# Optimization experiments

Measured on AMD Instinct MI355X. Metric: run time of the kernel, lower is better.

The kernel has to match this reference:

```python
import jax, jax.numpy as jnp
import numpy as np


def setup_inputs() -> dict:
    key = jax.random.key(0)
    k1, k2, k3 = jax.random.split(key, 3)
    B, L, H = 4, 4096, 1024
    x = jax.random.normal(k1, (B, L, H), dtype=jnp.float32)
    # 0.02 scale keeps attention logits in a sane range (like trained weights)
    in_proj_weight = jax.random.normal(k2, (3 * H, H), dtype=jnp.float32) * 0.02
    in_proj_bias = jnp.zeros((3 * H,), dtype=jnp.float32)
    out_proj_weight = jax.random.normal(k3, (H, H), dtype=jnp.float32) * 0.02
    out_proj_bias = jnp.zeros((H,), dtype=jnp.float32)
    return {
        "x": x,
        "in_proj_weight": in_proj_weight,
        "in_proj_bias": in_proj_bias,
        "out_proj_weight": out_proj_weight,
        "out_proj_bias": out_proj_bias,
        "num_heads": 16,
        "window_size": 128,
    }


def _windowed_mha(x, in_proj_weight, in_proj_bias, out_proj_weight, out_proj_bias,
                  num_heads, window_size):
    B, L, H = x.shape
    P = window_size
    pad = (-L) % P  # static
    xp = jnp.pad(x, ((0, 0), (0, pad), (0, 0))) if pad else x
    Lp = xp.shape[1]
    nw = Lp // P
    w = xp.reshape(B * nw, P, H)  # [NW, P, H]
    # packed QKV projection (torch MHA: q,k,v = split(x @ W_in.T + b_in))
    qkv = jnp.einsum('nph,dh->npd', w, in_proj_weight) + in_proj_bias
    q, k, v = jnp.split(qkv, 3, axis=-1)
    hd = H // num_heads

    def to_heads(t):
        return t.reshape(B * nw, P, num_heads, hd).transpose(0, 2, 1, 3)  # [NW, Hh, P, hd]

    q, k, v = to_heads(q), to_heads(k), to_heads(v)
    scale = 1.0 / jnp.sqrt(jnp.asarray(hd, dtype=x.dtype))
    scores = jnp.einsum('nhqd,nhkd->nhqk', q * scale, k)  # [NW, Hh, P, P]
    attn = jax.nn.softmax(scores, axis=-1)
    o = jnp.einsum('nhqk,nhkd->nhqd', attn, v)  # [NW, Hh, P, hd]
    o = o.transpose(0, 2, 1, 3).reshape(B * nw, P, H)
    o = jnp.einsum('nph,oh->npo', o, out_proj_weight) + out_proj_bias
    o = o.reshape(B, Lp, H)
    return o[:, :L]


def reference(x, in_proj_weight, in_proj_bias, out_proj_weight, out_proj_bias,
              num_heads, window_size):
    return _windowed_mha(x, in_proj_weight, in_proj_bias, out_proj_weight,
                         out_proj_bias, num_heads, window_size)
```

## Files before the change

### kernel.cpp

```cpp
#include <hip/hip_runtime.h>
#include <hip/hip_bf16.h>
#include <cstdint>


typedef __bf16 bf16_t;
typedef __bf16 bf16x8 __attribute__((ext_vector_type(8)));
typedef __bf16 bf16x4 __attribute__((ext_vector_type(4)));
typedef float  floatx4 __attribute__((ext_vector_type(4)));

#define MFMA_16x16x32(A, B, C) __builtin_amdgcn_mfma_f32_16x16x32_bf16(A, B, C, 0, 0, 0)

__device__ __forceinline__ void gld_lds16(const bf16_t* g, bf16_t* l) {
  __builtin_amdgcn_global_load_lds(
      (__attribute__((address_space(1))) void*)(void*)(g),
      (__attribute__((address_space(3))) void*)(l), 16, 0, 0);
}

__global__ void cvt_f32_to_bf16(const float* __restrict__ src,
                                bf16_t* __restrict__ dst, int n8) {
  int i = blockIdx.x * blockDim.x + threadIdx.x;
  if (i >= n8) return;
  const float4* s4 = (const float4*)src;
  float4 a = s4[2 * (size_t)i];
  float4 b = s4[2 * (size_t)i + 1];
  bf16x8 o;
  o[0] = (bf16_t)a.x; o[1] = (bf16_t)a.y; o[2] = (bf16_t)a.z; o[3] = (bf16_t)a.w;
  o[4] = (bf16_t)b.x; o[5] = (bf16_t)b.y; o[6] = (bf16_t)b.z; o[7] = (bf16_t)b.w;
  *(bf16x8*)(dst + (size_t)i * 8) = o;
}

__global__ void cvt_repack_win(const float* __restrict__ Win,
                               bf16_t* __restrict__ Wpk) {
  const int dr = blockIdx.x;
  const int head = dr / 192, s = dr - head * 192;
  const int src = (s < 64) ? head * 64 + s
                : (s < 128) ? 1024 + head * 64 + (s - 64)
                            : 2048 + head * 64 + (s - 128);
  const float4* srow = (const float4*)(Win + (size_t)src * 1024);
  const int i = threadIdx.x;
  float4 a = srow[2 * i];
  float4 b = srow[2 * i + 1];
  bf16x8 o;
  o[0] = (bf16_t)a.x; o[1] = (bf16_t)a.y; o[2] = (bf16_t)a.z; o[3] = (bf16_t)a.w;
  o[4] = (bf16_t)b.x; o[5] = (bf16_t)b.y; o[6] = (bf16_t)b.z; o[7] = (bf16_t)b.w;
  *(bf16x8*)(Wpk + (size_t)dr * 1024 + i * 8) = o;
}

template <bool F32OUT>
__global__ __launch_bounds__(256, 3) void gemm_bt(
    const bf16_t* __restrict__ A, const bf16_t* __restrict__ Bm,
    const float* __restrict__ bias, void* __restrict__ Cp,
    int M, int N, int K) {
  __shared__ bf16_t As[128 * 64];
  __shared__ bf16_t Bs[128 * 64];
  const int tid  = threadIdx.x;
  const int lane = tid & 63;
  const int wave = tid >> 6;
  const int n16  = lane & 15;
  const int q4   = lane >> 4;
  const int wm   = (wave >> 1) * 64;
  const int wn   = (wave & 1) * 64;
  const int m0   = blockIdx.y * 128;
  const int n0   = blockIdx.x * 128;

  floatx4 acc[4][4] = {};

  for (int k0 = 0; k0 < K; k0 += 64) {
    __syncthreads();
#pragma unroll
    for (int it = 0; it < 4; ++it) {
      const int ch = it * 256 + tid;
      const int r  = ch >> 3;
      const int c8 = (ch & 7) ^ (r & 7);
      gld_lds16(A  + (size_t)(m0 + r) * K + k0 + c8 * 8,
                As + (it * 256 + wave * 64) * 8);
      gld_lds16(Bm + (size_t)(n0 + r) * K + k0 + c8 * 8,
                Bs + (it * 256 + wave * 64) * 8);
    }
    __syncthreads();

#pragma unroll
    for (int half = 0; half < 2; ++half) {
      bf16x8 af[4], bfr[4];
#pragma unroll
      for (int i = 0; i < 4; ++i) {
        const int row = wm + i * 16 + n16;
        af[i] = *(const bf16x8*)&As[row * 64 + (((half * 4 + q4) ^ (row & 7)) * 8)];
      }
#pragma unroll
      for (int j = 0; j < 4; ++j) {
        const int row = wn + j * 16 + n16;
        bfr[j] = *(const bf16x8*)&Bs[row * 64 + (((half * 4 + q4) ^ (row & 7)) * 8)];
      }
#pragma unroll
      for (int i = 0; i < 4; ++i)
#pragma unroll
        for (int j = 0; j < 4; ++j)
          acc[i][j] = MFMA_16x16x32(af[i], bfr[j], acc[i][j]);
    }
  }

#pragma unroll
  for (int i = 0; i < 4; ++i)
#pragma unroll
    for (int j = 0; j < 4; ++j) {
      const int col = n0 + wn + j * 16 + n16;
      const float b = bias[col];
#pragma unroll
      for (int r = 0; r < 4; ++r) {
        const int row = m0 + wm + i * 16 + q4 * 4 + r;
        const float v = acc[i][j][r] + b;
        if (F32OUT)
          ((float*)Cp)[(size_t)row * N + col] = v;
        else
          ((bf16_t*)Cp)[(size_t)row * N + col] = (bf16_t)v;
      }
    }
}

__global__ __launch_bounds__(256, 3) void qkv_attn(
    const bf16_t* __restrict__ X,
    const bf16_t* __restrict__ Wpk,
    const float* __restrict__ bin,
    bf16_t* __restrict__ o)
{
  __shared__ bf16_t smem[26624];
  bf16_t* Xs  = smem;
  bf16_t* Ws  = smem + 8192;
  bf16_t* qs  = smem;
  bf16_t* ks  = smem + 9216;
  bf16_t* vsT = smem + 18432;
  bf16_t* Ps  = smem;

  const int wid  = blockIdx.x;
  const int h    = blockIdx.y;
  const int tid  = threadIdx.x;
  const int lane = tid & 63;
  const int wave = tid >> 6;
  const int n16  = lane & 15;
  const int q4   = lane >> 4;
  const int wm   = (wave >> 1) * 64;
  const int wn   = (wave & 1) * 96;

  const bf16_t* Xg = X + (size_t)wid * 128 * 1024;
  const bf16_t* Wg = Wpk + (size_t)h * 192 * 1024;

  floatx4 acc[4][6] = {};
  for (int k0 = 0; k0 < 1024; k0 += 64) {
    __syncthreads();
#pragma unroll
    for (int it = 0; it < 4; ++it) {
      const int ch = it * 256 + tid;
      const int r  = ch >> 3;
      const int c8 = (ch & 7) ^ (r & 7);
      gld_lds16(Xg + (size_t)r * 1024 + k0 + c8 * 8,
                Xs + (it * 256 + wave * 64) * 8);
    }
#pragma unroll
    for (int it = 0; it < 6; ++it) {
      const int ch = it * 256 + tid;
      const int r  = ch >> 3;
      const int c8 = (ch & 7) ^ (r & 7);
      gld_lds16(Wg + (size_t)r * 1024 + k0 + c8 * 8,
                Ws + (it * 256 + wave * 64) * 8);
    }
    __syncthreads();

#pragma unroll
    for (int half = 0; half < 2; ++half) {
      bf16x8 af[4], bfr[6];
#pragma unroll
      for (int i = 0; i < 4; ++i) {
        const int row = wm + i * 16 + n16;
        af[i] = *(const bf16x8*)&Xs[row * 64 + (((half * 4 + q4) ^ (row & 7)) * 8)];
      }
#pragma unroll
      for (int j = 0; j < 6; ++j) {
        const int row = wn + j * 16 + n16;
        bfr[j] = *(const bf16x8*)&Ws[row * 64 + (((half * 4 + q4) ^ (row & 7)) * 8)];
      }
#pragma unroll
      for (int i = 0; i < 4; ++i)
#pragma unroll
        for (int j = 0; j < 6; ++j)
          acc[i][j] = MFMA_16x16x32(af[i], bfr[j], acc[i][j]);
    }
  }
  __syncthreads();

#pragma unroll
  for (int j = 0; j < 6; ++j) {
    const int base = wn + j * 16;
    const int col  = base + n16;
    const int gb = (base < 64) ? h * 64 + col
                 : (base < 128) ? 1024 + h * 64 + (col - 64)
                                : 2048 + h * 64 + (col - 128);
    const float bias = bin[gb];
#pragma unroll
    for (int i = 0; i < 4; ++i) {
      const int row0 = wm + i * 16 + q4 * 4;
      if (base < 64) {
#pragma unroll
        for (int r = 0; r < 4; ++r)
          qs[(row0 + r) * 72 + col] = (bf16_t)((acc[i][j][r] + bias) * 0.125f);
      } else if (base < 128) {
#pragma unroll
        for (int r = 0; r < 4; ++r)
          ks[(row0 + r) * 72 + (col - 64)] = (bf16_t)(acc[i][j][r] + bias);
      } else {
        bf16x4 pv;
#pragma unroll
        for (int r = 0; r < 4; ++r) pv[r] = (bf16_t)(acc[i][j][r] + bias);
        const int d = col - 128;
        const int c8 = row0 >> 3, pos = row0 & 7;
        *(bf16x4*)&vsT[d * 128 + ((c8 ^ n16) << 3) + pos] = pv;
      }
    }
  }
  __syncthreads();

  floatx4 sacc[2][8] = {};
#pragma unroll
  for (int ks0 = 0; ks0 < 2; ++ks0) {
    bf16x8 aq[2];
#pragma unroll
    for (int i = 0; i < 2; ++i)
      aq[i] = *(const bf16x8*)&qs[(wave * 32 + i * 16 + n16) * 72 + ks0 * 32 + q4 * 8];
#pragma unroll
    for (int j = 0; j < 8; ++j) {
      bf16x8 bk = *(const bf16x8*)&ks[(j * 16 + n16) * 72 + ks0 * 32 + q4 * 8];
      sacc[0][j] = MFMA_16x16x32(aq[0], bk, sacc[0][j]);
      sacc[1][j] = MFMA_16x16x32(aq[1], bk, sacc[1][j]);
    }
  }
  __syncthreads();

  float invs[2][4];
#pragma unroll
  for (int i = 0; i < 2; ++i) {
#pragma unroll
    for (int r = 0; r < 4; ++r) {
      float vals[8];
      float s = 0.f;
#pragma unroll
      for (int j = 0; j < 8; ++j) {
        vals[j] = __expf(sacc[i][j][r]);
        s += vals[j];
      }
      for (int m = 1; m < 16; m <<= 1) s += __shfl_xor(s, m, 64);
      invs[i][r] = 1.0f / s;
      const int prow = wave * 32 + i * 16 + q4 * 4 + r;
#pragma unroll
      for (int j = 0; j < 8; ++j)
        Ps[prow * 136 + j * 16 + n16] = (bf16_t)vals[j];
    }
  }
  __syncthreads();

  floatx4 oacc[2][4] = {};
#pragma unroll
  for (int kk = 0; kk < 4; ++kk) {
    bf16x8 ap[2];
#pragma unroll
    for (int i = 0; i < 2; ++i)
      ap[i] = *(const bf16x8*)&Ps[(wave * 32 + i * 16 + n16) * 136 + kk * 32 + q4 * 8];
#pragma unroll
    for (int j = 0; j < 4; ++j) {
      const int d = j * 16 + n16;
      bf16x8 bv = *(const bf16x8*)&vsT[d * 128 + (((kk * 4 + q4) ^ n16) << 3)];
      oacc[0][j] = MFMA_16x16x32(ap[0], bv, oacc[0][j]);
      oacc[1][j] = MFMA_16x16x32(ap[1], bv, oacc[1][j]);
    }
  }

  bf16_t* go = o + (size_t)wid * 128 * 1024 + h * 64;
#pragma unroll
  for (int i = 0; i < 2; ++i)
#pragma unroll
    for (int j = 0; j < 4; ++j)
#pragma unroll
      for (int r = 0; r < 4; ++r) {
        const int row = wave * 32 + i * 16 + q4 * 4 + r;
        go[(size_t)row * 1024 + j * 16 + n16] = (bf16_t)(oacc[i][j][r] * invs[i][r]);
      }
}

extern "C" void kernel_launch(void* const* d_in, const int* in_sizes, int n_in,
                              void* d_out, int out_size, void* d_ws, size_t ws_size,
                              hipStream_t stream) {
  const float* x    = (const float*)d_in[0];
  const float* Win  = (const float*)d_in[1];
  const float* bin  = (const float*)d_in[2];
  const float* Wout = (const float*)d_in[3];
  const float* bout = (const float*)d_in[4];
  float* out = (float*)d_out;

  const size_t M = 16384, H = 1024, H3 = 3072;

  bf16_t* xb    = (bf16_t*)d_ws;
  bf16_t* Wpk   = xb + M * H;
  bf16_t* Woutb = Wpk + H3 * H;
  bf16_t* ob    = Woutb + H * H;

  cvt_f32_to_bf16<<<dim3((unsigned)(M * H / 8 / 256)), 256, 0, stream>>>(
      x, xb, (int)(M * H / 8));
  cvt_repack_win<<<dim3((unsigned)H3), 128, 0, stream>>>(Win, Wpk);
  cvt_f32_to_bf16<<<dim3((unsigned)(H * H / 8 / 256)), 256, 0, stream>>>(
      Wout, Woutb, (int)(H * H / 8));

  qkv_attn<<<dim3(128, 16), 256, 0, stream>>>(xb, Wpk, bin, ob);

  gemm_bt<true><<<dim3((unsigned)(H / 128), (unsigned)(M / 128)), 256, 0, stream>>>(
      ob, Woutb, bout, out, (int)M, (int)H, (int)H);
}
```

Baseline: 291.3 us.

## Merge conversion kernels into one launch and widen out-projection GEMM tile

The three fp32-to-bf16 conversion and repack kernels are folded into a single launch that dispatches on the global thread index, removing two kernel launches and their tail effects. The output-projection GEMM now uses a 128x256 tile, with each wave computing 64x128, so A-tile reuse doubles and fewer blocks re-read A. In exchange, accumulator registers double and occupancy drops to 2 blocks per CU, and only 4x128 = 512 blocks are launched, which may underfill the GPU.

After: 281.7 us. -3.3%, faster.

```diff
diff --git a/kernel.cpp b/kernel.cpp
--- a/kernel.cpp
+++ b/kernel.cpp
@@ -16,54 +16,56 @@
       (__attribute__((address_space(3))) void*)(l), 16, 0, 0);
 }
 
-__global__ void cvt_f32_to_bf16(const float* __restrict__ src,
-                                bf16_t* __restrict__ dst, int n8) {
-  int i = blockIdx.x * blockDim.x + threadIdx.x;
-  if (i >= n8) return;
-  const float4* s4 = (const float4*)src;
-  float4 a = s4[2 * (size_t)i];
-  float4 b = s4[2 * (size_t)i + 1];
+__device__ __forceinline__ void cvt8(const float* __restrict__ s,
+                                     bf16_t* __restrict__ d) {
+  float4 a = ((const float4*)s)[0];
+  float4 b = ((const float4*)s)[1];
   bf16x8 o;
   o[0] = (bf16_t)a.x; o[1] = (bf16_t)a.y; o[2] = (bf16_t)a.z; o[3] = (bf16_t)a.w;
   o[4] = (bf16_t)b.x; o[5] = (bf16_t)b.y; o[6] = (bf16_t)b.z; o[7] = (bf16_t)b.w;
-  *(bf16x8*)(dst + (size_t)i * 8) = o;
-}
-
-__global__ void cvt_repack_win(const float* __restrict__ Win,
-                               bf16_t* __restrict__ Wpk) {
-  const int dr = blockIdx.x;
-  const int head = dr / 192, s = dr - head * 192;
-  const int src = (s < 64) ? head * 64 + s
-                : (s < 128) ? 1024 + head * 64 + (s - 64)
-                            : 2048 + head * 64 + (s - 128);
-  const float4* srow = (const float4*)(Win + (size_t)src * 1024);
-  const int i = threadIdx.x;
-  float4 a = srow[2 * i];
-  float4 b = srow[2 * i + 1];
-  bf16x8 o;
-  o[0] = (bf16_t)a.x; o[1] = (bf16_t)a.y; o[2] = (bf16_t)a.z; o[3] = (bf16_t)a.w;
-  o[4] = (bf16_t)b.x; o[5] = (bf16_t)b.y; o[6] = (bf16_t)b.z; o[7] = (bf16_t)b.w;
-  *(bf16x8*)(Wpk + (size_t)dr * 1024 + i * 8) = o;
-}
-
-template <bool F32OUT>
-__global__ __launch_bounds__(256, 3) void gemm_bt(
+  *(bf16x8*)d = o;
+}
+
+__global__ void cvt_all(const float* __restrict__ x,
+                        const float* __restrict__ Win,
+                        const float* __restrict__ Wout,
+                        bf16_t* __restrict__ xb,
+                        bf16_t* __restrict__ Wpk,
+                        bf16_t* __restrict__ Woutb) {
+  const int idx = blockIdx.x * 256 + threadIdx.x;
+  if (idx < 2097152) {
+    cvt8(x + (size_t)idx * 8, xb + (size_t)idx * 8);
+  } else if (idx < 2228224) {
+    const int i = idx - 2097152;
+    cvt8(Wout + (size_t)i * 8, Woutb + (size_t)i * 8);
+  } else {
+    const int c = idx - 2228224;
+    const int dr = c >> 7, i = c & 127;
+    const int head = dr / 192, s = dr - head * 192;
+    const int src = (s < 64) ? head * 64 + s
+                  : (s < 128) ? 1024 + head * 64 + (s - 64)
+                              : 2048 + head * 64 + (s - 128);
+    cvt8(Win + (size_t)src * 1024 + i * 8, Wpk + (size_t)dr * 1024 + i * 8);
+  }
+}
+
+__global__ __launch_bounds__(256, 2) void gemm_out(
     const bf16_t* __restrict__ A, const bf16_t* __restrict__ Bm,
-    const float* __restrict__ bias, void* __restrict__ Cp,
+    const float* __restrict__ bias, float* __restrict__ C,
     int M, int N, int K) {
   __shared__ bf16_t As[128 * 64];
-  __shared__ bf16_t Bs[128 * 64];
+  __shared__ bf16_t Bs[256 * 64];
   const int tid  = threadIdx.x;
   const int lane = tid & 63;
   const int wave = tid >> 6;
   const int n16  = lane & 15;
   const int q4   = lane >> 4;
   const int wm   = (wave >> 1) * 64;
-  const int wn   = (wave & 1) * 64;
+  const int wn   = (wave & 1) * 128;
   const int m0   = blockIdx.y * 128;
-  const int n0   = blockIdx.x * 128;
-
-  floatx4 acc[4][4] = {};
+  const int n0   = blockIdx.x * 256;
+
+  floatx4 acc[4][8] = {};
 
   for (int k0 = 0; k0 < K; k0 += 64) {
     __syncthreads();
@@ -72,8 +74,14 @@
       const int ch = it * 256 + tid;
       const int r  = ch >> 3;
       const int c8 = (ch & 7) ^ (r & 7);
-      gld_lds16(A  + (size_t)(m0 + r) * K + k0 + c8 * 8,
+      gld_lds16(A + (size_t)(m0 + r) * K + k0 + c8 * 8,
                 As + (it * 256 + wave * 64) * 8);
+    }
+#pragma unroll
+    for (int it = 0; it < 8; ++it) {
+      const int ch = it * 256 + tid;
+      const int r  = ch >> 3;
+      const int c8 = (ch & 7) ^ (r & 7);
       gld_lds16(Bm + (size_t)(n0 + r) * K + k0 + c8 * 8,
                 Bs + (it * 256 + wave * 64) * 8);
     }
@@ -81,21 +89,21 @@
 
 #pragma unroll
     for (int half = 0; half < 2; ++half) {
-      bf16x8 af[4], bfr[4];
+      bf16x8 af[4], bfr[8];
 #pragma unroll
       for (int i = 0; i < 4; ++i) {
         const int row = wm + i * 16 + n16;
         af[i] = *(const bf16x8*)&As[row * 64 + (((half * 4 + q4) ^ (row & 7)) * 8)];
       }
 #pragma unroll
-      for (int j = 0; j < 4; ++j) {
+      for (int j = 0; j < 8; ++j) {
         const int row = wn + j * 16 + n16;
         bfr[j] = *(const bf16x8*)&Bs[row * 64 + (((half * 4 + q4) ^ (row & 7)) * 8)];
       }
 #pragma unroll
       for (int i = 0; i < 4; ++i)
 #pragma unroll
-        for (int j = 0; j < 4; ++j)
+        for (int j = 0; j < 8; ++j)
           acc[i][j] = MFMA_16x16x32(af[i], bfr[j], acc[i][j]);
     }
   }
@@ -103,17 +111,13 @@
 #pragma unroll
   for (int i = 0; i < 4; ++i)
 #pragma unroll
-    for (int j = 0; j < 4; ++j) {
+    for (int j = 0; j < 8; ++j) {
       const int col = n0 + wn + j * 16 + n16;
       const float b = bias[col];
 #pragma unroll
       for (int r = 0; r < 4; ++r) {
         const int row = m0 + wm + i * 16 + q4 * 4 + r;
-        const float v = acc[i][j][r] + b;
-        if (F32OUT)
-          ((float*)Cp)[(size_t)row * N + col] = v;
-        else
-          ((bf16_t*)Cp)[(size_t)row * N + col] = (bf16_t)v;
+        C[(size_t)row * N + col] = acc[i][j][r] + b;
       }
     }
 }
@@ -302,14 +306,10 @@
   bf16_t* Woutb = Wpk + H3 * H;
   bf16_t* ob    = Woutb + H * H;
 
-  cvt_f32_to_bf16<<<dim3((unsigned)(M * H / 8 / 256)), 256, 0, stream>>>(
-      x, xb, (int)(M * H / 8));
-  cvt_repack_win<<<dim3((unsigned)H3), 128, 0, stream>>>(Win, Wpk);
-  cvt_f32_to_bf16<<<dim3((unsigned)(H * H / 8 / 256)), 256, 0, stream>>>(
-      Wout, Woutb, (int)(H * H / 8));
+  cvt_all<<<dim3(10240), 256, 0, stream>>>(x, Win, Wout, xb, Wpk, Woutb);
 
   qkv_attn<<<dim3(128, 16), 256, 0, stream>>>(xb, Wpk, bin, ob);
 
-  gemm_bt<true><<<dim3((unsigned)(H / 128), (unsigned)(M / 128)), 256, 0, stream>>>(
+  gemm_out<<<dim3((unsigned)(H / 256), (unsigned)(M / 128)), 256, 0, stream>>>(
       ob, Woutb, bout, out, (int)M, (int)H, (int)H);
 }
```
